# Performance work log

Hardware: AMD Instinct MI355X
Metric: run time of the kernel (lower is better)

The kernel has to match this reference:

```python
import jax, jax.numpy as jnp
import numpy as np

WS = 7        # window_size
SHIFT = 3     # shift_size
HEADS = 6
DIM = 192
HIDDEN = DIM * 6  # mlp_ratio=6
EPS = 1e-5


def _rel_pos_index(ws):
    # static relative-position index, (ws*ws, ws*ws) int
    coords = np.stack(np.meshgrid(np.arange(ws), np.arange(ws), indexing='ij')).reshape(2, -1)
    rel = coords[:, :, None] - coords[:, None, :]            # (2, N, N)
    rel = rel.transpose(1, 2, 0)                             # (N, N, 2)
    rel[:, :, 0] += ws - 1
    rel[:, :, 1] += ws - 1
    rel[:, :, 0] *= 2 * ws - 1
    return rel.sum(-1)


def _layernorm(t, g, b):
    m = t.mean(-1, keepdims=True)
    v = jnp.mean((t - m) ** 2, axis=-1, keepdims=True)
    return (t - m) * jax.lax.rsqrt(v + EPS) * g + b


def setup_inputs() -> dict:
    key = jax.random.key(0)
    ks = jax.random.split(key, 8)
    B, H, W = 16, 56, 56
    x = jax.random.normal(ks[0], (B, H * W, DIM), dtype=jnp.float32)
    p = lambda k, s: (jax.random.normal(k, s, dtype=jnp.float32) * 0.02)
    return {
        'x': x, 'H': H, 'W': W,
        'ln1_g': jnp.ones((DIM,), jnp.float32), 'ln1_b': jnp.zeros((DIM,), jnp.float32),
        'qkv_w': p(ks[1], (3 * DIM, DIM)), 'qkv_b': jnp.zeros((3 * DIM,), jnp.float32),
        'rpb': p(ks[2], ((2 * WS - 1) ** 2, HEADS)),
        'proj_w': p(ks[3], (DIM, DIM)), 'proj_b': jnp.zeros((DIM,), jnp.float32),
        'ln2_g': jnp.ones((DIM,), jnp.float32), 'ln2_b': jnp.zeros((DIM,), jnp.float32),
        'fc1_w': p(ks[4], (HIDDEN, DIM)), 'fc1_b': jnp.zeros((HIDDEN,), jnp.float32),
        'fc2_w': p(ks[5], (DIM, HIDDEN)), 'fc2_b': jnp.zeros((DIM,), jnp.float32),
    }


def reference(x, H, W, ln1_g, ln1_b, qkv_w, qkv_b, rpb, proj_w, proj_b,
              ln2_g, ln2_b, fc1_w, fc1_b, fc2_w, fc2_b):
    B, L, C = x.shape
    hd = C // HEADS
    shortcut = x
    h = _layernorm(x, ln1_g, ln1_b).reshape(B, H, W, C)
    pad_r = (WS - W % WS) % WS
    pad_b = (WS - H % WS) % WS
    h = jnp.pad(h, ((0, 0), (0, pad_b), (0, pad_r), (0, 0)))
    Hp, Wp = H + pad_b, W + pad_r
    if SHIFT > 0:
        h = jnp.roll(h, (-SHIFT, -SHIFT), axis=(1, 2))
    # window partition -> (nW*B, WS*WS, C)
    h = h.reshape(B, Hp // WS, WS, Wp // WS, WS, C).transpose(0, 1, 3, 2, 4, 5)
    h = h.reshape(-1, WS * WS, C)
    nB, N, _ = h.shape
    qkv = (h @ qkv_w.T + qkv_b).reshape(nB, N, 3, HEADS, hd).transpose(2, 0, 3, 1, 4)
    q, k, v = qkv[0], qkv[1], qkv[2]       # (nB, heads, N, hd)
    scale = hd ** -0.5
    attn = jnp.einsum('bhnd,bhmd->bhnm', q * scale, k)
    idx = _rel_pos_index(WS)
    bias = rpb[idx.reshape(-1)].reshape(N, N, HEADS).transpose(2, 0, 1)  # (heads, N, N)
    attn = jax.nn.softmax(attn + bias[None], axis=-1)
    out = jnp.einsum('bhnm,bhmd->bhnd', attn, v).transpose(0, 2, 1, 3).reshape(nB, N, C)
    out = out @ proj_w.T + proj_b
    # window reverse -> (B, Hp, Wp, C)
    out = out.reshape(B, Hp // WS, Wp // WS, WS, WS, C).transpose(0, 1, 3, 2, 4, 5)
    out = out.reshape(B, Hp, Wp, C)
    if SHIFT > 0:
        out = jnp.roll(out, (SHIFT, SHIFT), axis=(1, 2))
    out = out[:, :H, :W, :].reshape(B, H * W, C)
    x = shortcut + out
    h2 = _layernorm(x, ln2_g, ln2_b)
    h2 = jax.nn.gelu(h2 @ fc1_w.T + fc1_b, approximate=False)
    return x + (h2 @ fc2_w.T + fc2_b)
```

## Files before the change

### kernel.cpp

```cpp
#include <hip/hip_runtime.h>

typedef unsigned short u16;
typedef __bf16 bf16x8 __attribute__((ext_vector_type(8)));
typedef __bf16 bf16x2_t __attribute__((ext_vector_type(2)));
typedef float f32x4 __attribute__((ext_vector_type(4)));

#define AS1 __attribute__((address_space(1)))
#define AS3 __attribute__((address_space(3)))

__device__ __forceinline__ void gld16(const void* g, void* l) {
  __builtin_amdgcn_global_load_lds((const AS1 void*)g, (AS3 void*)l, 16, 0, 0);
}

__device__ __forceinline__ u16 f2bf(float f) {
  union { float f; unsigned int u; } v; v.f = f;
  unsigned int u = v.u;
  u += 0x7fffu + ((u >> 16) & 1u);
  return (u16)(u >> 16);
}
__device__ __forceinline__ float bf2f(u16 h) {
  union { unsigned int u; float f; } v; v.u = ((unsigned int)h) << 16; return v.f;
}
__device__ __forceinline__ unsigned int pk2(float a, float b) {
#if __has_builtin(__builtin_amdgcn_cvt_pk_bf16_f32)
  union { bf16x2_t v; unsigned int u; } c;
  c.v = __builtin_amdgcn_cvt_pk_bf16_f32(a, b);
  return c.u;
#else
  return (unsigned int)f2bf(a) | ((unsigned int)f2bf(b) << 16);
#endif
}
__device__ __forceinline__ float gelu_f(float v) {
  float u = v * (1.5957691216f + 0.0713548163f * v * v);
  return v * __builtin_amdgcn_rcpf(1.0f + __expf(-u));
}

__global__ __launch_bounds__(256) void cast_weights(
    const float* __restrict__ w0, const float* __restrict__ w1,
    const float* __restrict__ w2, const float* __restrict__ w3,
    u16* __restrict__ o0, u16* __restrict__ o1,
    u16* __restrict__ o2, u16* __restrict__ o3) {
  int i = blockIdx.x * 256 + threadIdx.x;
  if (i < 110592) o0[i] = f2bf(w0[i]);
  if (i < 36864) {
    int n = i / 192, kp = i - n * 192;
    int h = kp >> 5, dp = kp & 31;
    int d = (dp & 1) ? ((dp >> 1) + 16) : (dp >> 1);
    o1[i] = f2bf(w1[n * 192 + h * 32 + d]);
  }
  if (i < 221184) o2[i] = f2bf(w2[i]);
  if (i < 221184) o3[i] = f2bf(w3[i]);
}

__global__ __launch_bounds__(256) void build_btab(
    const float* __restrict__ rpb, float* __restrict__ btab) {
  int id = blockIdx.x * 256 + threadIdx.x;
  int head = id >> 12;
  int m = (id >> 6) & 63;
  int r = id & 63;
  float v;
  if (m >= 49) v = -1e30f;
  else if (r >= 49) v = 0.0f;
  else {
    int mi = m / 7, mj = m - mi * 7;
    int ri = r / 7, rj = r - ri * 7;
    v = rpb[((ri - mi + 6) * 13 + (rj - mj + 6)) * 6 + head];
  }
  btab[id] = v;
}

__global__ __launch_bounds__(256) void ln_kernel(
    const float* __restrict__ x, const float* __restrict__ g,
    const float* __restrict__ b, u16* __restrict__ out) {
  int row = blockIdx.x * 4 + (threadIdx.x >> 6);
  int lane = threadIdx.x & 63;
  const float* xr = x + (long)row * 192;
  float e0 = xr[lane], e1 = xr[lane + 64], e2 = xr[lane + 128];
  float s = e0 + e1 + e2;
  #pragma unroll
  for (int o = 1; o < 64; o <<= 1) s += __shfl_xor(s, o);
  float mean = s * (1.0f / 192.0f);
  float d0 = e0 - mean, d1 = e1 - mean, d2 = e2 - mean;
  float q = d0 * d0 + d1 * d1 + d2 * d2;
  #pragma unroll
  for (int o = 1; o < 64; o <<= 1) q += __shfl_xor(q, o);
  float rstd = rsqrtf(q * (1.0f / 192.0f) + 1e-5f);
  u16* orow = out + (long)row * 192;
  orow[lane]       = f2bf(d0 * rstd * g[lane]       + b[lane]);
  orow[lane + 64]  = f2bf(d1 * rstd * g[lane + 64]  + b[lane + 64]);
  orow[lane + 128] = f2bf(d2 * rstd * g[lane + 128] + b[lane + 128]);
}

template<int MODE>
__global__ __launch_bounds__(256, 3) void gemm_kernel(
    const u16* __restrict__ A, const u16* __restrict__ W,
    const float* __restrict__ bias, const float* __restrict__ resid,
    void* __restrict__ out, int N, int K) {
  __shared__ u16 lds[25600];
  float* ct = (float*)lds;
  const int tid = threadIdx.x;
  const int wave = tid >> 6, lane = tid & 63;
  const int wm = wave >> 1, wn = wave & 1;
  const int quad = lane >> 4, l15 = lane & 15;
  const long bm = (long)blockIdx.x * 128;
  const int bn = blockIdx.y * 96;

  f32x4 acc[4][3] = {};
  for (int kc = 0; kc < K; kc += 96) {
    if (kc) __syncthreads();
    for (int t = wave; t < 42; t += 4) {
      int isB = t >= 24;
      int tt = isB ? t - 24 : t;
      int grp = tt / 3, kt = tt - grp * 3;
      const u16* g = isB
          ? (W + (long)(bn + grp * 16 + l15) * K + kc + kt * 32 + quad * 8)
          : (A + (bm + grp * 16 + l15) * K + kc + kt * 32 + quad * 8);
      gld16(g, &lds[(isB ? 12288 : 0) + tt * 512]);
    }
    __syncthreads();
    #pragma unroll
    for (int kt = 0; kt < 3; kt++) {
      bf16x8 af[4], bfr[3];
      #pragma unroll
      for (int mt = 0; mt < 4; mt++)
        af[mt] = *(const bf16x8*)&lds[((wm * 4 + mt) * 3 + kt) * 512 + lane * 8];
      #pragma unroll
      for (int nt = 0; nt < 3; nt++)
        bfr[nt] = *(const bf16x8*)&lds[12288 + ((wn * 3 + nt) * 3 + kt) * 512 + lane * 8];
      #pragma unroll
      for (int mt = 0; mt < 4; mt++)
        #pragma unroll
        for (int nt = 0; nt < 3; nt++)
          acc[mt][nt] = __builtin_amdgcn_mfma_f32_16x16x32_bf16(af[mt], bfr[nt], acc[mt][nt], 0, 0, 0);
    }
  }
  __syncthreads();
  #pragma unroll
  for (int nt = 0; nt < 3; nt++) {
    int col = wn * 48 + nt * 16 + l15;
    float bi = bias[bn + col];
    #pragma unroll
    for (int mt = 0; mt < 4; mt++) {
      int row0 = wm * 64 + mt * 16 + quad * 4;
      #pragma unroll
      for (int j = 0; j < 4; j++)
        ct[(row0 + j) * 100 + col] = acc[mt][nt][j] + bi;
    }
  }
  __syncthreads();
  #pragma unroll
  for (int it = 0; it < 12; it++) {
    int c = it * 256 + tid;
    int row = c / 24, i = c - row * 24;
    float4 v = *(const float4*)&ct[row * 100 + i * 4];
    long idx = (bm + row) * (long)N + bn + i * 4;
    if (MODE == 2) {
      const float4 rv = *(const float4*)(resid + idx);
      v.x += rv.x; v.y += rv.y; v.z += rv.z; v.w += rv.w;
      *(float4*)((float*)out + idx) = v;
    } else {
      if (MODE == 1) {
        v.x = gelu_f(v.x); v.y = gelu_f(v.y); v.z = gelu_f(v.z); v.w = gelu_f(v.w);
      }
      uint2 pk;
      pk.x = pk2(v.x, v.y);
      pk.y = pk2(v.z, v.w);
      *(uint2*)((u16*)out + idx) = pk;
    }
  }
}

__global__ __launch_bounds__(256) void attn_kernel(
    const u16* __restrict__ qkv, const float* __restrict__ btab,
    u16* __restrict__ attn) {
  __shared__ u16 lds[4 * 7040];
  int tid = threadIdx.x;
  int wave = tid >> 6, lane = tid & 63;
  int quad = lane >> 4, l15 = lane & 15;
  int w = blockIdx.x * 4 + wave;
  int win = w / 6, head = w - win * 6;
  int b = win >> 6, wy = (win >> 3) & 7, wx = win & 7;
  u16* lp = lds + wave * 7040;
  u16* lvt = lp + 4608;
  float* rsum = (float*)(lp + 6912);

  bf16x8 qb[4], ka[4];
  #pragma unroll
  for (int t = 0; t < 4; t++) {
    int n = t * 16 + l15;
    uint4 qv = {0, 0, 0, 0}, kv = {0, 0, 0, 0}, vv = {0, 0, 0, 0};
    if (n < 49) {
      int i = n / 7, j = n - i * 7;
      int y = wy * 7 + i + 3;  if (y >= 56) y -= 56;
      int xx = wx * 7 + j + 3; if (xx >= 56) xx -= 56;
      long base = ((long)(b * 3136 + y * 56 + xx)) * 576 + head * 32 + quad * 8;
      qv = *(const uint4*)(qkv + base);
      kv = *(const uint4*)(qkv + base + 192);
      vv = *(const uint4*)(qkv + base + 384);
    }
    qb[t] = *(const bf16x8*)&qv;
    ka[t] = *(const bf16x8*)&kv;
    const u16* vp = (const u16*)&vv;
    #pragma unroll
    for (int d = 0; d < 8; d++) lvt[(quad * 8 + d) * 72 + n] = vp[d];
  }

  f32x4 s[4][4];
  const f32x4 fz = {0.0f, 0.0f, 0.0f, 0.0f};
  #pragma unroll
  for (int tm = 0; tm < 4; tm++)
    #pragma unroll
    for (int tr = 0; tr < 4; tr++)
      s[tm][tr] = __builtin_amdgcn_mfma_f32_16x16x32_bf16(ka[tm], qb[tr], fz, 0, 0, 0);

  const float scale = 0.17677669529663687f;
  const float* bt = btab + head * 4096;
  float mx[4] = {-1e30f, -1e30f, -1e30f, -1e30f};
  #pragma unroll
  for (int tm = 0; tm < 4; tm++) {
    int m0 = tm * 16 + quad * 4;
    #pragma unroll
    for (int tr = 0; tr < 4; tr++) {
      int r = tr * 16 + l15;
      #pragma unroll
      for (int j = 0; j < 4; j++) {
        float v = s[tm][tr][j] * scale + bt[(m0 + j) * 64 + r];
        s[tm][tr][j] = v;
        mx[tr] = fmaxf(mx[tr], v);
      }
    }
  }
  #pragma unroll
  for (int tr = 0; tr < 4; tr++) {
    mx[tr] = fmaxf(mx[tr], __shfl_xor(mx[tr], 16));
    mx[tr] = fmaxf(mx[tr], __shfl_xor(mx[tr], 32));
  }
  float sm[4] = {0.f, 0.f, 0.f, 0.f};
  #pragma unroll
  for (int tm = 0; tm < 4; tm++) {
    #pragma unroll
    for (int tr = 0; tr < 4; tr++) {
      int r = tr * 16 + l15;
      float e0 = __expf(s[tm][tr][0] - mx[tr]);
      float e1 = __expf(s[tm][tr][1] - mx[tr]);
      float e2 = __expf(s[tm][tr][2] - mx[tr]);
      float e3 = __expf(s[tm][tr][3] - mx[tr]);
      sm[tr] += (e0 + e1) + (e2 + e3);
      uint2 pk;
      pk.x = pk2(e0, e1);
      pk.y = pk2(e2, e3);
      *(uint2*)&lp[r * 72 + tm * 16 + quad * 4] = pk;
    }
  }
  #pragma unroll
  for (int tr = 0; tr < 4; tr++) {
    sm[tr] += __shfl_xor(sm[tr], 16);
    sm[tr] += __shfl_xor(sm[tr], 32);
  }
  if (quad == 0) {
    #pragma unroll
    for (int tr = 0; tr < 4; tr++) rsum[tr * 16 + l15] = __builtin_amdgcn_rcpf(sm[tr]);
  }

  f32x4 o[4][2] = {};
  #pragma unroll
  for (int ks = 0; ks < 2; ks++) {
    bf16x8 vb0 = *(const bf16x8*)&lvt[(l15) * 72 + ks * 32 + quad * 8];
    bf16x8 vb1 = *(const bf16x8*)&lvt[(16 + l15) * 72 + ks * 32 + quad * 8];
    #pragma unroll
    for (int rt = 0; rt < 4; rt++) {
      bf16x8 pf = *(const bf16x8*)&lp[(rt * 16 + l15) * 72 + ks * 32 + quad * 8];
      o[rt][0] = __builtin_amdgcn_mfma_f32_16x16x32_bf16(pf, vb0, o[rt][0], 0, 0, 0);
      o[rt][1] = __builtin_amdgcn_mfma_f32_16x16x32_bf16(pf, vb1, o[rt][1], 0, 0, 0);
    }
  }
  #pragma unroll
  for (int rt = 0; rt < 4; rt++) {
    #pragma unroll
    for (int j = 0; j < 4; j++) {
      int r = rt * 16 + quad * 4 + j;
      if (r < 49) {
        float inv = rsum[r];
        int i = r / 7, jj = r - i * 7;
        int y = wy * 7 + i + 3;   if (y >= 56) y -= 56;
        int xx = wx * 7 + jj + 3; if (xx >= 56) xx -= 56;
        long base = ((long)(b * 3136 + y * 56 + xx)) * 192 + head * 32 + 2 * l15;
        *(unsigned int*)&attn[base] = pk2(o[rt][0][j] * inv, o[rt][1][j] * inv);
      }
    }
  }
}

extern "C" void kernel_launch(void* const* d_in, const int* in_sizes, int n_in,
                              void* d_out, int out_size, void* d_ws, size_t ws_size,
                              hipStream_t stream) {
  (void)in_sizes; (void)n_in; (void)out_size; (void)ws_size;
  const float* x      = (const float*)d_in[0];
  const float* ln1_g  = (const float*)d_in[3];
  const float* ln1_b  = (const float*)d_in[4];
  const float* qkv_w  = (const float*)d_in[5];
  const float* qkv_b  = (const float*)d_in[6];
  const float* rpb    = (const float*)d_in[7];
  const float* proj_w = (const float*)d_in[8];
  const float* proj_b = (const float*)d_in[9];
  const float* ln2_g  = (const float*)d_in[10];
  const float* ln2_b  = (const float*)d_in[11];
  const float* fc1_w  = (const float*)d_in[12];
  const float* fc1_b  = (const float*)d_in[13];
  const float* fc2_w  = (const float*)d_in[14];
  const float* fc2_b  = (const float*)d_in[15];

  char* ws = (char*)d_ws;
  float* x2   = (float*)(ws + 0);
  u16* hA     = (u16*)(ws + 38535168);
  float* btab = (float*)(ws + 38535168);
  u16* qkv    = (u16*)(ws + 57802752);
  u16* attn   = (u16*)(ws + 115605504);
  u16* hid    = (u16*)(ws + 57802752);
  u16* wbuf   = (u16*)(ws + 173408256);
  u16* qkv_wb  = wbuf;
  u16* proj_wb = wbuf + 110592;
  u16* fc1_wb  = wbuf + 147456;
  u16* fc2_wb  = wbuf + 368640;

  cast_weights<<<dim3(864), 256, 0, stream>>>(qkv_w, proj_w, fc1_w, fc2_w,
                                              qkv_wb, proj_wb, fc1_wb, fc2_wb);
  ln_kernel<<<dim3(12544), 256, 0, stream>>>(x, ln1_g, ln1_b, hA);
  gemm_kernel<0><<<dim3(392, 6), 256, 0, stream>>>(hA, qkv_wb, qkv_b, nullptr,
                                                   qkv, 576, 192);
  build_btab<<<dim3(96), 256, 0, stream>>>(rpb, btab);
  attn_kernel<<<dim3(1536), 256, 0, stream>>>(qkv, btab, attn);
  gemm_kernel<2><<<dim3(392, 2), 256, 0, stream>>>(attn, proj_wb, proj_b, x,
                                                   x2, 192, 192);
  ln_kernel<<<dim3(12544), 256, 0, stream>>>(x2, ln2_g, ln2_b, hA);
  gemm_kernel<1><<<dim3(392, 12), 256, 0, stream>>>(hA, fc1_wb, fc1_b, nullptr,
                                                    hid, 1152, 192);
  gemm_kernel<2><<<dim3(392, 2), 256, 0, stream>>>(hid, fc2_wb, fc2_b, x2,
                                                   (float*)d_out, 192, 1152);
}
```

Measured before the change: 352.9 us.

## Fuse fc1+GELU+fc2 MLP into one kernel keeping hidden activations on-chip

Replaces the separate fc1 (with GELU) and fc2 GEMM launches with a single fused MLP kernel. Each wave processes 32 rows, computes 96-wide hidden chunks with MFMA, applies bias and GELU, and stages the bf16 result in LDS. It then accumulates that chunk directly into the fc2 output registers. This removes the global write and read of the large hidden tensor and one launch. In exchange, weights are read straight from global memory with no LDS tiling, so each wave re-reads the full W1 and W2, and the 128-thread blocks with many accumulators may limit occupancy.

```diff
diff --git a/kernel.cpp b/kernel.cpp
--- a/kernel.cpp
+++ b/kernel.cpp
@@ -159,13 +159,82 @@
       v.x += rv.x; v.y += rv.y; v.z += rv.z; v.w += rv.w;
       *(float4*)((float*)out + idx) = v;
     } else {
-      if (MODE == 1) {
-        v.x = gelu_f(v.x); v.y = gelu_f(v.y); v.z = gelu_f(v.z); v.w = gelu_f(v.w);
-      }
       uint2 pk;
       pk.x = pk2(v.x, v.y);
       pk.y = pk2(v.z, v.w);
       *(uint2*)((u16*)out + idx) = pk;
+    }
+  }
+}
+
+__global__ __launch_bounds__(128, 2) void mlp_kernel(
+    const u16* __restrict__ hA, const u16* __restrict__ W1,
+    const float* __restrict__ b1, const u16* __restrict__ W2,
+    const float* __restrict__ b2, const float* __restrict__ x2,
+    float* __restrict__ out) {
+  __shared__ u16 lds[2 * 3072];
+  const int tid = threadIdx.x;
+  const int wave = tid >> 6, lane = tid & 63;
+  const int quad = lane >> 4, l15 = lane & 15;
+  u16* hx = lds + wave * 3072;
+  const long R = ((long)blockIdx.x * 2 + wave) * 32;
+
+  f32x4 acc2[2][12] = {};
+  for (int nc = 0; nc < 12; nc++) {
+    f32x4 acc1[6][2] = {};
+    #pragma unroll
+    for (int kt = 0; kt < 6; kt++) {
+      bf16x8 a0 = *(const bf16x8*)(hA + (R + l15) * 192 + kt * 32 + quad * 8);
+      bf16x8 a1 = *(const bf16x8*)(hA + (R + 16 + l15) * 192 + kt * 32 + quad * 8);
+      #pragma unroll
+      for (int ctt = 0; ctt < 6; ctt++) {
+        bf16x8 w1f = *(const bf16x8*)(W1 + (long)(nc * 96 + ctt * 16 + l15) * 192 + kt * 32 + quad * 8);
+        acc1[ctt][0] = __builtin_amdgcn_mfma_f32_16x16x32_bf16(w1f, a0, acc1[ctt][0], 0, 0, 0);
+        acc1[ctt][1] = __builtin_amdgcn_mfma_f32_16x16x32_bf16(w1f, a1, acc1[ctt][1], 0, 0, 0);
+      }
+    }
+    #pragma unroll
+    for (int ctt = 0; ctt < 6; ctt++) {
+      float4 bb = *(const float4*)(b1 + nc * 96 + ctt * 16 + quad * 4);
+      #pragma unroll
+      for (int rt = 0; rt < 2; rt++) {
+        float g0 = gelu_f(acc1[ctt][rt][0] + bb.x);
+        float g1 = gelu_f(acc1[ctt][rt][1] + bb.y);
+        float g2 = gelu_f(acc1[ctt][rt][2] + bb.z);
+        float g3 = gelu_f(acc1[ctt][rt][3] + bb.w);
+        uint2 pk;
+        pk.x = pk2(g0, g1);
+        pk.y = pk2(g2, g3);
+        int addr = (rt * 3 + (ctt >> 1)) * 512 + ((ctt & 1) * 2 + (quad >> 1)) * 128
+                 + l15 * 8 + (quad & 1) * 4;
+        *(uint2*)&hx[addr] = pk;
+      }
+    }
+    #pragma unroll
+    for (int kt2 = 0; kt2 < 3; kt2++) {
+      bf16x8 h0 = *(const bf16x8*)&hx[kt2 * 512 + lane * 8];
+      bf16x8 h1 = *(const bf16x8*)&hx[(3 + kt2) * 512 + lane * 8];
+      #pragma unroll
+      for (int nt = 0; nt < 12; nt++) {
+        bf16x8 w2f = *(const bf16x8*)(W2 + (long)(nt * 16 + l15) * 1152 + nc * 96 + kt2 * 32 + quad * 8);
+        acc2[0][nt] = __builtin_amdgcn_mfma_f32_16x16x32_bf16(w2f, h0, acc2[0][nt], 0, 0, 0);
+        acc2[1][nt] = __builtin_amdgcn_mfma_f32_16x16x32_bf16(w2f, h1, acc2[1][nt], 0, 0, 0);
+      }
+    }
+  }
+  #pragma unroll
+  for (int nt = 0; nt < 12; nt++) {
+    float4 bb = *(const float4*)(b2 + nt * 16 + quad * 4);
+    #pragma unroll
+    for (int rt = 0; rt < 2; rt++) {
+      long idx = (R + rt * 16 + l15) * 192 + nt * 16 + quad * 4;
+      float4 rv = *(const float4*)(x2 + idx);
+      float4 v;
+      v.x = acc2[rt][nt][0] + bb.x + rv.x;
+      v.y = acc2[rt][nt][1] + bb.y + rv.y;
+      v.z = acc2[rt][nt][2] + bb.z + rv.z;
+      v.w = acc2[rt][nt][3] + bb.w + rv.w;
+      *(float4*)(out + idx) = v;
     }
   }
 }
@@ -316,7 +385,6 @@
   float* btab = (float*)(ws + 38535168);
   u16* qkv    = (u16*)(ws + 57802752);
   u16* attn   = (u16*)(ws + 115605504);
-  u16* hid    = (u16*)(ws + 57802752);
   u16* wbuf   = (u16*)(ws + 173408256);
   u16* qkv_wb  = wbuf;
   u16* proj_wb = wbuf + 110592;
@@ -333,8 +401,6 @@
   gemm_kernel<2><<<dim3(392, 2), 256, 0, stream>>>(attn, proj_wb, proj_b, x,
                                                    x2, 192, 192);
   ln_kernel<<<dim3(12544), 256, 0, stream>>>(x2, ln2_g, ln2_b, hA);
-  gemm_kernel<1><<<dim3(392, 12), 256, 0, stream>>>(hA, fc1_wb, fc1_b, nullptr,
-                                                    hid, 1152, 192);
-  gemm_kernel<2><<<dim3(392, 2), 256, 0, stream>>>(hid, fc2_wb, fc2_b, x2,
-                                                   (float*)d_out, 192, 1152);
-}
+  mlp_kernel<<<dim3(784), 128, 0, stream>>>(hA, fc1_wb, fc1_b, fc2_wb, fc2_b,
+                                            x2, (float*)d_out);
+}
```

Result: slower. 425.1 us (+20.4%).

## Double-buffer GEMM K-chunks in LDS and split epilogue to shrink shared memory

Applied to the files above, without the earlier changes.

Replaces the single-buffered 96-wide K chunk loop with a double-buffered 32-wide pipeline, so the async global->LDS load of the next chunk overlaps the MFMAs on the current one. The epilogue now stages the output tile in two 64-row halves, which cuts LDS use from about 51KB to 28KB and raises the launch_bounds occupancy hint from 3 to 4. In exchange there is one barrier per 32-wide K step instead of per 96, which may add sync overhead. It also relies on the gld16 completion being covered by __syncthreads.

```diff
diff --git a/kernel.cpp b/kernel.cpp
--- a/kernel.cpp
+++ b/kernel.cpp
@@ -92,11 +92,11 @@
 }
 
 template<int MODE>
-__global__ __launch_bounds__(256, 3) void gemm_kernel(
+__global__ __launch_bounds__(256, 4) void gemm_kernel(
     const u16* __restrict__ A, const u16* __restrict__ W,
     const float* __restrict__ bias, const float* __restrict__ resid,
     void* __restrict__ out, int N, int K) {
-  __shared__ u16 lds[25600];
+  __shared__ u16 lds[2 * 7168];
   float* ct = (float*)lds;
   const int tid = threadIdx.x;
   const int wave = tid >> 6, lane = tid & 63;
@@ -104,69 +104,83 @@
   const int quad = lane >> 4, l15 = lane & 15;
   const long bm = (long)blockIdx.x * 128;
   const int bn = blockIdx.y * 96;
+  const int NC = K >> 5;
+
+  for (int t = wave; t < 14; t += 4) {
+    const u16* g = (t < 8)
+        ? (A + (bm + t * 16 + l15) * K + quad * 8)
+        : (W + (long)(bn + (t - 8) * 16 + l15) * K + quad * 8);
+    gld16(g, &lds[t * 512]);
+  }
+  __syncthreads();
 
   f32x4 acc[4][3] = {};
-  for (int kc = 0; kc < K; kc += 96) {
-    if (kc) __syncthreads();
-    for (int t = wave; t < 42; t += 4) {
-      int isB = t >= 24;
-      int tt = isB ? t - 24 : t;
-      int grp = tt / 3, kt = tt - grp * 3;
-      const u16* g = isB
-          ? (W + (long)(bn + grp * 16 + l15) * K + kc + kt * 32 + quad * 8)
-          : (A + (bm + grp * 16 + l15) * K + kc + kt * 32 + quad * 8);
-      gld16(g, &lds[(isB ? 12288 : 0) + tt * 512]);
-    }
-    __syncthreads();
-    #pragma unroll
-    for (int kt = 0; kt < 3; kt++) {
-      bf16x8 af[4], bfr[3];
-      #pragma unroll
-      for (int mt = 0; mt < 4; mt++)
-        af[mt] = *(const bf16x8*)&lds[((wm * 4 + mt) * 3 + kt) * 512 + lane * 8];
+  for (int c = 0; c < NC; c++) {
+    const int cur = c & 1;
+    if (c + 1 < NC) {
+      const int kof = (c + 1) * 32 + quad * 8;
+      const int nb = (cur ^ 1) * 7168;
+      for (int t = wave; t < 14; t += 4) {
+        const u16* g = (t < 8)
+            ? (A + (bm + t * 16 + l15) * K + kof)
+            : (W + (long)(bn + (t - 8) * 16 + l15) * K + kof);
+        gld16(g, &lds[nb + t * 512]);
+      }
+    }
+    const u16* buf = lds + cur * 7168;
+    bf16x8 af[4], bfr[3];
+    #pragma unroll
+    for (int mt = 0; mt < 4; mt++)
+      af[mt] = *(const bf16x8*)&buf[(wm * 4 + mt) * 512 + lane * 8];
+    #pragma unroll
+    for (int nt = 0; nt < 3; nt++)
+      bfr[nt] = *(const bf16x8*)&buf[(8 + wn * 3 + nt) * 512 + lane * 8];
+    #pragma unroll
+    for (int mt = 0; mt < 4; mt++)
       #pragma unroll
       for (int nt = 0; nt < 3; nt++)
-        bfr[nt] = *(const bf16x8*)&lds[12288 + ((wn * 3 + nt) * 3 + kt) * 512 + lane * 8];
+        acc[mt][nt] = __builtin_amdgcn_mfma_f32_16x16x32_bf16(af[mt], bfr[nt], acc[mt][nt], 0, 0, 0);
+    __syncthreads();
+  }
+
+  #pragma unroll
+  for (int h = 0; h < 2; h++) {
+    if (wm == h) {
       #pragma unroll
-      for (int mt = 0; mt < 4; mt++)
+      for (int nt = 0; nt < 3; nt++) {
+        int col = wn * 48 + nt * 16 + l15;
+        float bi = bias[bn + col];
         #pragma unroll
-        for (int nt = 0; nt < 3; nt++)
-          acc[mt][nt] = __builtin_amdgcn_mfma_f32_16x16x32_bf16(af[mt], bfr[nt], acc[mt][nt], 0, 0, 0);
-    }
-  }
-  __syncthreads();
-  #pragma unroll
-  for (int nt = 0; nt < 3; nt++) {
-    int col = wn * 48 + nt * 16 + l15;
-    float bi = bias[bn + col];
-    #pragma unroll
-    for (int mt = 0; mt < 4; mt++) {
-      int row0 = wm * 64 + mt * 16 + quad * 4;
-      #pragma unroll
-      for (int j = 0; j < 4; j++)
-        ct[(row0 + j) * 100 + col] = acc[mt][nt][j] + bi;
-    }
-  }
-  __syncthreads();
-  #pragma unroll
-  for (int it = 0; it < 12; it++) {
-    int c = it * 256 + tid;
-    int row = c / 24, i = c - row * 24;
-    float4 v = *(const float4*)&ct[row * 100 + i * 4];
-    long idx = (bm + row) * (long)N + bn + i * 4;
-    if (MODE == 2) {
-      const float4 rv = *(const float4*)(resid + idx);
-      v.x += rv.x; v.y += rv.y; v.z += rv.z; v.w += rv.w;
-      *(float4*)((float*)out + idx) = v;
-    } else {
-      if (MODE == 1) {
-        v.x = gelu_f(v.x); v.y = gelu_f(v.y); v.z = gelu_f(v.z); v.w = gelu_f(v.w);
-      }
-      uint2 pk;
-      pk.x = pk2(v.x, v.y);
-      pk.y = pk2(v.z, v.w);
-      *(uint2*)((u16*)out + idx) = pk;
-    }
+        for (int mt = 0; mt < 4; mt++) {
+          int row0 = mt * 16 + quad * 4;
+          #pragma unroll
+          for (int j = 0; j < 4; j++)
+            ct[(row0 + j) * 100 + col] = acc[mt][nt][j] + bi;
+        }
+      }
+    }
+    __syncthreads();
+    #pragma unroll
+    for (int it = 0; it < 6; it++) {
+      int cc = it * 256 + tid;
+      int row = cc / 24, i = cc - row * 24;
+      float4 v = *(const float4*)&ct[row * 100 + i * 4];
+      long idx = (bm + h * 64 + row) * (long)N + bn + i * 4;
+      if (MODE == 2) {
+        const float4 rv = *(const float4*)(resid + idx);
+        v.x += rv.x; v.y += rv.y; v.z += rv.z; v.w += rv.w;
+        *(float4*)((float*)out + idx) = v;
+      } else {
+        if (MODE == 1) {
+          v.x = gelu_f(v.x); v.y = gelu_f(v.y); v.z = gelu_f(v.z); v.w = gelu_f(v.w);
+        }
+        uint2 pk;
+        pk.x = pk2(v.x, v.y);
+        pk.y = pk2(v.z, v.w);
+        *(uint2*)((u16*)out + idx) = pk;
+      }
+    }
+    if (h == 0) __syncthreads();
   }
 }
 
```

After: 341.9 us. 1.03x faster.

## Replace 4-wave GEMM with single-wave double-buffered GEMM using async LDS loads

Applied to the files above, without the earlier changes.

Replaces the 256-thread GEMM that uses 128x96 tiles and K chunks of 96 with a 64-thread single-wave kernel on 64x48 tiles. K is processed in 32-wide chunks, and global_load_lds prefetches the next chunk into a second LDS buffer while the MFMAs run on the current one. A waitcnt replaces the block barriers. The aim is to overlap loads with compute and raise the block count for occupancy. The cost is smaller tiles, so operands are reloaded more often from global memory and each block has fewer MFMAs. The epilogue also reuses LDS without a barrier after the last async loads, which relies on ordering within a single wave.

```diff
diff --git a/kernel.cpp b/kernel.cpp
--- a/kernel.cpp
+++ b/kernel.cpp
@@ -92,68 +92,71 @@
 }
 
 template<int MODE>
-__global__ __launch_bounds__(256, 3) void gemm_kernel(
+__global__ __launch_bounds__(64) void wgemm(
     const u16* __restrict__ A, const u16* __restrict__ W,
     const float* __restrict__ bias, const float* __restrict__ resid,
     void* __restrict__ out, int N, int K) {
-  __shared__ u16 lds[25600];
+  __shared__ u16 lds[2 * 3584];
   float* ct = (float*)lds;
-  const int tid = threadIdx.x;
-  const int wave = tid >> 6, lane = tid & 63;
-  const int wm = wave >> 1, wn = wave & 1;
+  const int lane = threadIdx.x;
   const int quad = lane >> 4, l15 = lane & 15;
-  const long bm = (long)blockIdx.x * 128;
-  const int bn = blockIdx.y * 96;
+  const long bm = (long)blockIdx.x * 64;
+  const int bn = blockIdx.y * 48;
+  const int NC = K >> 5;
+
+  const u16* ga[7];
+  #pragma unroll
+  for (int t = 0; t < 7; t++)
+    ga[t] = (t < 4)
+        ? (A + (bm + t * 16 + l15) * K + quad * 8)
+        : (W + (long)(bn + (t - 4) * 16 + l15) * K + quad * 8);
+
+  #pragma unroll
+  for (int t = 0; t < 7; t++) gld16(ga[t], &lds[t * 512]);
 
   f32x4 acc[4][3] = {};
-  for (int kc = 0; kc < K; kc += 96) {
-    if (kc) __syncthreads();
-    for (int t = wave; t < 42; t += 4) {
-      int isB = t >= 24;
-      int tt = isB ? t - 24 : t;
-      int grp = tt / 3, kt = tt - grp * 3;
-      const u16* g = isB
-          ? (W + (long)(bn + grp * 16 + l15) * K + kc + kt * 32 + quad * 8)
-          : (A + (bm + grp * 16 + l15) * K + kc + kt * 32 + quad * 8);
-      gld16(g, &lds[(isB ? 12288 : 0) + tt * 512]);
-    }
-    __syncthreads();
-    #pragma unroll
-    for (int kt = 0; kt < 3; kt++) {
-      bf16x8 af[4], bfr[3];
+  for (int c = 0; c < NC; c++) {
+    const int cur = c & 1;
+    const u16* buf = lds + cur * 3584;
+    __builtin_amdgcn_s_waitcnt(0x0F70);
+    bf16x8 af[4], bfr[3];
+    #pragma unroll
+    for (int mt = 0; mt < 4; mt++)
+      af[mt] = *(const bf16x8*)&buf[mt * 512 + lane * 8];
+    #pragma unroll
+    for (int nt = 0; nt < 3; nt++)
+      bfr[nt] = *(const bf16x8*)&buf[(4 + nt) * 512 + lane * 8];
+    if (c + 1 < NC) {
+      const int kof = (c + 1) * 32;
+      const int nb = (cur ^ 1) * 3584;
       #pragma unroll
-      for (int mt = 0; mt < 4; mt++)
-        af[mt] = *(const bf16x8*)&lds[((wm * 4 + mt) * 3 + kt) * 512 + lane * 8];
+      for (int t = 0; t < 7; t++) gld16(ga[t] + kof, &lds[nb + t * 512]);
+    }
+    #pragma unroll
+    for (int mt = 0; mt < 4; mt++)
       #pragma unroll
       for (int nt = 0; nt < 3; nt++)
-        bfr[nt] = *(const bf16x8*)&lds[12288 + ((wn * 3 + nt) * 3 + kt) * 512 + lane * 8];
-      #pragma unroll
-      for (int mt = 0; mt < 4; mt++)
-        #pragma unroll
-        for (int nt = 0; nt < 3; nt++)
-          acc[mt][nt] = __builtin_amdgcn_mfma_f32_16x16x32_bf16(af[mt], bfr[nt], acc[mt][nt], 0, 0, 0);
-    }
-  }
-  __syncthreads();
+        acc[mt][nt] = __builtin_amdgcn_mfma_f32_16x16x32_bf16(af[mt], bfr[nt], acc[mt][nt], 0, 0, 0);
+  }
+
   #pragma unroll
   for (int nt = 0; nt < 3; nt++) {
-    int col = wn * 48 + nt * 16 + l15;
+    int col = nt * 16 + l15;
     float bi = bias[bn + col];
     #pragma unroll
     for (int mt = 0; mt < 4; mt++) {
-      int row0 = wm * 64 + mt * 16 + quad * 4;
+      int row0 = mt * 16 + quad * 4;
       #pragma unroll
       for (int j = 0; j < 4; j++)
-        ct[(row0 + j) * 100 + col] = acc[mt][nt][j] + bi;
-    }
-  }
-  __syncthreads();
+        ct[(row0 + j) * 49 + col] = acc[mt][nt][j] + bi;
+    }
+  }
   #pragma unroll
   for (int it = 0; it < 12; it++) {
-    int c = it * 256 + tid;
-    int row = c / 24, i = c - row * 24;
-    float4 v = *(const float4*)&ct[row * 100 + i * 4];
-    long idx = (bm + row) * (long)N + bn + i * 4;
+    int flat = it * 64 + lane;
+    int row = flat / 12, gcol = (flat - row * 12) * 4;
+    float4 v = *(const float4*)&ct[row * 49 + gcol];
+    long idx = (bm + row) * (long)N + bn + gcol;
     if (MODE == 2) {
       const float4 rv = *(const float4*)(resid + idx);
       v.x += rv.x; v.y += rv.y; v.z += rv.z; v.w += rv.w;
@@ -326,15 +329,15 @@
   cast_weights<<<dim3(864), 256, 0, stream>>>(qkv_w, proj_w, fc1_w, fc2_w,
                                               qkv_wb, proj_wb, fc1_wb, fc2_wb);
   ln_kernel<<<dim3(12544), 256, 0, stream>>>(x, ln1_g, ln1_b, hA);
-  gemm_kernel<0><<<dim3(392, 6), 256, 0, stream>>>(hA, qkv_wb, qkv_b, nullptr,
-                                                   qkv, 576, 192);
+  wgemm<0><<<dim3(784, 12), 64, 0, stream>>>(hA, qkv_wb, qkv_b, nullptr,
+                                             qkv, 576, 192);
   build_btab<<<dim3(96), 256, 0, stream>>>(rpb, btab);
   attn_kernel<<<dim3(1536), 256, 0, stream>>>(qkv, btab, attn);
-  gemm_kernel<2><<<dim3(392, 2), 256, 0, stream>>>(attn, proj_wb, proj_b, x,
-                                                   x2, 192, 192);
+  wgemm<2><<<dim3(784, 4), 64, 0, stream>>>(attn, proj_wb, proj_b, x,
+                                            x2, 192, 192);
   ln_kernel<<<dim3(12544), 256, 0, stream>>>(x2, ln2_g, ln2_b, hA);
-  gemm_kernel<1><<<dim3(392, 12), 256, 0, stream>>>(hA, fc1_wb, fc1_b, nullptr,
-                                                    hid, 1152, 192);
-  gemm_kernel<2><<<dim3(392, 2), 256, 0, stream>>>(hid, fc2_wb, fc2_b, x2,
-                                                   (float*)d_out, 192, 1152);
-}
+  wgemm<1><<<dim3(784, 24), 64, 0, stream>>>(hA, fc1_wb, fc1_b, nullptr,
+                                             hid, 1152, 192);
+  wgemm<2><<<dim3(784, 4), 64, 0, stream>>>(hid, fc2_wb, fc2_b, x2,
+                                            (float*)d_out, 192, 1152);
+}
```

Result: slower. 445.7 us (+26.3%).
